# Kernel tuning notes

Hardware: AMD Instinct MI355X
Metric: run time of the kernel (lower is better)

Reference implementation:

```python
import jax, jax.numpy as jnp
import numpy as np

N_ROW = 50000
N_COL = 50000
E = 600000
D = 128
NEG_SLOPE = 0.01  # torch LeakyReLU default


def _leaky(x):
    return jnp.where(x >= 0, x, NEG_SLOPE * x)


def _mlp(x, W1, b1, W2, b2):
    # (Linear -> LeakyReLU) x2, matching nn.Sequential in Conv_layer
    h = _leaky(x @ W1 + b1)
    return _leaky(h @ W2 + b2)


def setup_inputs() -> dict:
    key = jax.random.key(0)
    ks = jax.random.split(key, 16)
    inp = {
        "feat_row": jax.random.normal(ks[0], (N_ROW, D), jnp.float32),
        "feat_col": jax.random.normal(ks[1], (N_COL, D), jnp.float32),
        "src_c2r": jax.random.randint(ks[2], (E,), 0, N_COL, jnp.int32),
        "dst_c2r": jax.random.randint(ks[3], (E,), 0, N_ROW, jnp.int32),
        "w_c2r": jax.random.uniform(ks[4], (E,), jnp.float32),
        "src_r2c": jax.random.randint(ks[5], (E,), 0, N_ROW, jnp.int32),
        "dst_r2c": jax.random.randint(ks[6], (E,), 0, N_COL, jnp.int32),
        "w_r2c": jax.random.uniform(ks[7], (E,), jnp.float32),
        "W1_c2r": jax.random.normal(ks[8], (D, D), jnp.float32) / np.sqrt(D),
        "b1_c2r": jax.random.normal(ks[9], (D,), jnp.float32) * 0.01,
        "W2_c2r": jax.random.normal(ks[10], (D, D), jnp.float32) / np.sqrt(D),
        "b2_c2r": jax.random.normal(ks[11], (D,), jnp.float32) * 0.01,
        "W1_r2c": jax.random.normal(ks[12], (D, D), jnp.float32) / np.sqrt(D),
        "b1_r2c": jax.random.normal(ks[13], (D,), jnp.float32) * 0.01,
        "W2_r2c": jax.random.normal(ks[14], (D, D), jnp.float32) / np.sqrt(D),
        "b2_r2c": jax.random.normal(ks[15], (D,), jnp.float32) * 0.01,
        "eps_c2r": jnp.zeros((), jnp.float32),  # DGL GINConv init_eps=0
        "eps_r2c": jnp.zeros((), jnp.float32),
    }
    return inp


def reference(feat_row, feat_col, src_c2r, dst_c2r, w_c2r, src_r2c, dst_r2c, w_r2c,
              W1_c2r, b1_c2r, W2_c2r, b2_c2r, W1_r2c, b1_r2c, W2_r2c, b2_r2c,
              eps_c2r, eps_r2c):
    # col -> row GINConv (edge-weighted sum aggregation)
    msg = feat_col[src_c2r] * w_c2r[:, None]                       # [E, D]
    agg_row = jax.ops.segment_sum(msg, dst_c2r, num_segments=N_ROW)
    h_row = _mlp((1.0 + eps_c2r) * feat_row + agg_row, W1_c2r, b1_c2r, W2_c2r, b2_c2r)
    # row -> col GINConv using updated row features
    msg2 = h_row[src_r2c] * w_r2c[:, None]                         # [E, D]
    agg_col = jax.ops.segment_sum(msg2, dst_r2c, num_segments=N_COL)
    h_col = _mlp((1.0 + eps_r2c) * feat_col + agg_col, W1_r2c, b1_r2c, W2_r2c, b2_r2c)
    # residual (use_residual=True): add pre-conv embeddings
    return h_row + feat_row, h_col + feat_col
```

## Files before the change

### kernel.cpp

```cpp
#include <hip/hip_runtime.h>
#include <hip/hip_bf16.h>

#define NROW 50000
#define NCOL 50000
#define DDIM 128
#define CAP  32

typedef __bf16 bf16_t;
typedef __bf16 bf16x2 __attribute__((ext_vector_type(2)));
typedef __bf16 bf16x8 __attribute__((ext_vector_type(8)));
typedef float  f32x4  __attribute__((ext_vector_type(4)));

__device__ __forceinline__ float lrelu(float v) { return v >= 0.f ? v : 0.01f * v; }

__device__ __forceinline__ float ldf(const void* p, size_t i, bool f) {
    return f ? ((const float*)p)[i] : (float)((const bf16_t*)p)[i];
}

__device__ __forceinline__ bool dtf(const int* flags, int fi) {
    return (fi == -1) ? true : (fi == -2) ? false : (flags[fi] != 0);
}

struct TensorTab { const void* p[18]; int n[18]; };

__global__ __launch_bounds__(256) void detect_zero(TensorTab T, int* flags,
                                                   int* z, int zn)
{
    const int tid = threadIdx.x;
    if (blockIdx.x >= 18) {
        int i = (blockIdx.x - 18) * 256 + tid;
        if (i < zn) z[i] = 0;
        return;
    }
    __shared__ int vb, vf;
    const int t = blockIdx.x;
    if (tid == 0) { vb = 0; vf = 0; }
    __syncthreads();
    const int n = T.n[t];
    const bool isFloatArr = (t != 2 && t != 3 && t != 5 && t != 6) && n >= 2;
    if (isFloatArr) {
        int nw = n / 2;
        int wi = (int)(((long long)tid * nw) >> 8);
        unsigned w = ((const unsigned*)T.p[t])[wi];
        unsigned low = w & 0xffffu;
        if (low) {
            int e = (int)((low >> 7) & 0xffu);
            if (e >= 90 && e <= 141) atomicAdd(&vb, 1);
            else                     atomicAdd(&vf, 1);
        }
    }
    __syncthreads();
    if (tid == 0) flags[t] = (isFloatArr && vf > vb) ? 1 : 0;
}

__device__ __forceinline__ void fill_edges(
    int e, const int* __restrict__ dst, const int* __restrict__ srcArr,
    const void* __restrict__ wArr, int nE, int* __restrict__ counts,
    int2* __restrict__ slots2, int* __restrict__ ovCnt,
    int* __restrict__ ovList, bool fW)
{
    if (e >= nE) return;
    int d = dst[e];
    int pos = atomicAdd(&counts[d], 1);
    if (pos < CAP) {
        int2 pk;
        pk.x = srcArr[e];
        pk.y = __float_as_int(ldf(wArr, e, fW));
        slots2[(size_t)d * CAP + pos] = pk;
    } else {
        int k = atomicAdd(ovCnt, 1);
        ovList[k] = e;
    }
}

struct WPtrs { const void* W[4]; int fi[4]; };

__device__ __forceinline__ void prep_one(WPtrs P, const int* flags,
                                         __bf16* wfp, int slot)
{
    if (slot >= 4 * 2048) return;
    int m = slot >> 11, sIdx = slot & 2047;
    bool f = flags[P.fi[m]] != 0;
    int l = sIdx & 63, combo = sIdx >> 6;
    int ct = combo >> 2, kk = combo & 3;
    int col  = ct * 16 + (l & 15);
    int krow = kk * 32 + (l >> 4) * 8;
    bf16x8 v;
#pragma unroll
    for (int j = 0; j < 8; ++j)
        v[j] = (__bf16)ldf(P.W[m], (size_t)(krow + j) * DDIM + col, f);
    ((bf16x8*)wfp)[slot] = v;
}

__device__ __forceinline__ void convert_one(const void* __restrict__ feat,
                                            __bf16* __restrict__ cbuf,
                                            int i, int n8, bool f)
{
    if (i >= n8) return;
    bf16x8 v;
    if (f) {
        f32x4 a = ((const f32x4*)feat)[i * 2];
        f32x4 c = ((const f32x4*)feat)[i * 2 + 1];
#pragma unroll
        for (int j = 0; j < 4; ++j) { v[j] = (__bf16)a[j]; v[j + 4] = (__bf16)c[j]; }
    } else {
        v = ((const bf16x8*)feat)[i];
    }
    ((bf16x8*)cbuf)[i] = v;
}

__global__ __launch_bounds__(1024) void prep_fill_i2(
    WPtrs P, const int* __restrict__ flags, __bf16* __restrict__ wfp,
    const void* __restrict__ feat, __bf16* __restrict__ cbuf, int n8,
    int fiFeat, int cb, int eb, int K7,
    const int* __restrict__ f_dst, const int* __restrict__ f_src,
    const void* __restrict__ f_w, int f_nE, int* __restrict__ f_counts,
    int2* __restrict__ f_slots2, int* __restrict__ f_ovCnt,
    int* __restrict__ f_ovList, int f_fiW)
{
    const int g = blockIdx.x;
    const int tid = threadIdx.x;
    if (g >= K7) {
        prep_one(P, flags, wfp, (g - K7) * 1024 + tid);
        return;
    }
    int grp = g / 7, rem = g % 7;
    if (rem < 4) {
        int b = grp * 4 + rem;
        if (b >= cb) return;
        convert_one(feat, cbuf, b * 1024 + tid, n8, dtf(flags, fiFeat));
    } else {
        int b = grp * 3 + (rem - 4);
        if (b >= eb) return;
        fill_edges(b * 1024 + tid, f_dst, f_src, f_w, f_nE, f_counts,
                   f_slots2, f_ovCnt, f_ovList, dtf(flags, f_fiW));
    }
}

__global__ __launch_bounds__(256) void segsum_fill_i(
    const __bf16* __restrict__ gsrc, const int* __restrict__ counts,
    const int2* __restrict__ slots2, float* __restrict__ agg, int nRows,
    const int* __restrict__ srcArr, const int* __restrict__ dstArr,
    const void* __restrict__ wArr, const int* __restrict__ ovList,
    const int* __restrict__ ovCount, const int* __restrict__ flags, int fiW,
    int segBlocks, int fillBlocks,
    const int* __restrict__ f_dst, const int* __restrict__ f_src,
    const void* __restrict__ f_w, int f_nE, int* __restrict__ f_counts,
    int2* __restrict__ f_slots2, int* __restrict__ f_ovCnt,
    int* __restrict__ f_ovList, int f_fiW)
{
    const int tid = threadIdx.x;
    int bid;
    if (f_dst) {
        int grp = (int)blockIdx.x / 7, rem = (int)blockIdx.x % 7;
        if (rem >= 4) {
            int b = grp * 3 + (rem - 4);
            if (b < fillBlocks)
                fill_edges(b * 256 + tid, f_dst, f_src, f_w, f_nE, f_counts,
                           f_slots2, f_ovCnt, f_ovList, dtf(flags, f_fiW));
            return;
        }
        bid = grp * 4 + rem;
        if (bid >= segBlocks) return;
    } else {
        bid = blockIdx.x;
        if (bid >= segBlocks) return;
    }

    int row = bid * 4 + (tid >> 6);
    if (row >= nRows) return;
    int lane = tid & 63;

    int cntRaw = counts[row];
    int cnt = cntRaw > CAP ? CAP : cntRaw;

    int sr = 0; float wv = 0.f;
    if (lane < cnt) {
        int2 pk = slots2[(size_t)row * CAP + lane];
        sr = pk.x;
        wv = __int_as_float(pk.y);
    }

    float2* ap = (float2*)(agg + (size_t)row * DDIM) + lane;
    float2 acc0 = {0.f, 0.f}, acc1 = {0.f, 0.f};

    const bf16x2* fb = (const bf16x2*)gsrc;
    int i = 0;
    for (; i + 4 <= cnt; i += 4) {
        int   a0 = __shfl(sr, i),     a1 = __shfl(sr, i + 1);
        int   a2 = __shfl(sr, i + 2), a3 = __shfl(sr, i + 3);
        float w0 = __shfl(wv, i),     w1 = __shfl(wv, i + 1);
        float w2 = __shfl(wv, i + 2), w3 = __shfl(wv, i + 3);
        bf16x2 v0 = fb[(size_t)a0 * 64 + lane];
        bf16x2 v1 = fb[(size_t)a1 * 64 + lane];
        bf16x2 v2 = fb[(size_t)a2 * 64 + lane];
        bf16x2 v3 = fb[(size_t)a3 * 64 + lane];
        acc0.x += (float)v0[0] * w0; acc0.y += (float)v0[1] * w0;
        acc1.x += (float)v1[0] * w1; acc1.y += (float)v1[1] * w1;
        acc0.x += (float)v2[0] * w2; acc0.y += (float)v2[1] * w2;
        acc1.x += (float)v3[0] * w3; acc1.y += (float)v3[1] * w3;
    }
    for (; i < cnt; ++i) {
        int   a0 = __shfl(sr, i);
        float w0 = __shfl(wv, i);
        bf16x2 v0 = fb[(size_t)a0 * 64 + lane];
        acc0.x += (float)v0[0] * w0; acc0.y += (float)v0[1] * w0;
    }
    if (cntRaw > CAP) {
        const bool fW = dtf(flags, fiW);
        int nOv = *ovCount;
        for (int k = 0; k < nOv; ++k) {
            int e = ovList[k];
            if (dstArr[e] == row) {
                int s = srcArr[e];
                float wf = ldf(wArr, e, fW);
                bf16x2 v = fb[(size_t)s * 64 + lane];
                acc0.x += (float)v[0] * wf; acc0.y += (float)v[1] * wf;
            }
        }
    }
    acc0.x += acc1.x; acc0.y += acc1.y;
    *ap = acc0;
}

template <bool RESIDUAL, bool HOUT>
__global__ __launch_bounds__(256) void mlp_cs(
    const void* __restrict__ feat, const float* __restrict__ agg,
    const void* __restrict__ b1, const void* __restrict__ b2,
    const void* __restrict__ epsp, float* __restrict__ out, int N,
    const int* __restrict__ flags, int fiFeat, int fiB1, int fiB2, int fiEps,
    const __bf16* __restrict__ pW1, const __bf16* __restrict__ pW2,
    __bf16* __restrict__ hout,
    int mblocks,
    const int* __restrict__ f_dst, const int* __restrict__ f_src,
    const void* __restrict__ f_w, int f_nE, int* __restrict__ f_counts,
    int2* __restrict__ f_slots2, int* __restrict__ f_ovCnt,
    int* __restrict__ f_ovList, int f_fiW)
{
    __shared__ alignas(16) __bf16 At[16 * 136];
    __shared__ alignas(16) __bf16 H1[16 * 136];

    const int tid = threadIdx.x;
    if (f_dst && (int)blockIdx.x >= mblocks) {
        int e = ((int)blockIdx.x - mblocks) * 256 + tid;
        fill_edges(e, f_dst, f_src, f_w, f_nE, f_counts, f_slots2,
                   f_ovCnt, f_ovList, dtf(flags, f_fiW));
        return;
    }

    const bool fF  = flags[fiFeat] != 0;
    const bool fB1 = flags[fiB1] != 0;
    const bool fB2 = flags[fiB2] != 0;
    const bool fE  = flags[fiEps] != 0;

    const int lane = tid & 63;
    const int wave = tid >> 6;
    const int quad = lane >> 4;
    const int r    = lane & 15;
    const int rowBase = blockIdx.x * 16;
    const float eps1 = 1.f + ldf(epsp, 0, fE);

    {
        int row = tid >> 4;
        int k0  = (tid & 15) * 8;
        int g   = rowBase + row;
        bf16x8 av;
        if (g < N) {
            size_t base = (size_t)g * DDIM + k0;
            const f32x4* gp = (const f32x4*)(agg + base);
            f32x4 g0 = gp[0], g1 = gp[1];
            if (fF) {
                const f32x4* fp = (const f32x4*)((const float*)feat + base);
                f32x4 f0 = fp[0], f1 = fp[1];
#pragma unroll
                for (int j = 0; j < 4; ++j) {
                    av[j]     = (__bf16)(f0[j] * eps1 + g0[j]);
                    av[j + 4] = (__bf16)(f1[j] * eps1 + g1[j]);
                }
            } else {
                bf16x8 fv = *(const bf16x8*)((const bf16_t*)feat + base);
#pragma unroll
                for (int j = 0; j < 4; ++j) {
                    av[j]     = (__bf16)((float)fv[j]     * eps1 + g0[j]);
                    av[j + 4] = (__bf16)((float)fv[j + 4] * eps1 + g1[j]);
                }
            }
        } else {
#pragma unroll
            for (int j = 0; j < 8; ++j) av[j] = (__bf16)0.f;
        }
        *(bf16x8*)&At[row * 136 + k0] = av;
    }
    __syncthreads();

    bf16x8 a[4];
#pragma unroll
    for (int kk = 0; kk < 4; ++kk)
        a[kk] = *(const bf16x8*)&At[r * 136 + kk * 32 + quad * 8];

    const int ct0 = wave * 2, ct1 = ct0 + 1;

    const bf16x8* pw1v = (const bf16x8*)pW1;
    bf16x8 wfa[4], wfb[4];
#pragma unroll
    for (int kk = 0; kk < 4; ++kk) {
        wfa[kk] = pw1v[(ct0 * 4 + kk) * 64 + lane];
        wfb[kk] = pw1v[(ct1 * 4 + kk) * 64 + lane];
    }
    float b1a = ldf(b1, ct0 * 16 + r, fB1);
    float b1b = ldf(b1, ct1 * 16 + r, fB1);

    {
        f32x4 acc = {0.f, 0.f, 0.f, 0.f};
#pragma unroll
        for (int kk = 0; kk < 4; ++kk)
            acc = __builtin_amdgcn_mfma_f32_16x16x32_bf16(a[kk], wfa[kk], acc, 0, 0, 0);
#pragma unroll
        for (int gg = 0; gg < 4; ++gg)
            H1[(quad * 4 + gg) * 136 + ct0 * 16 + r] = (__bf16)lrelu(acc[gg] + b1a);
    }
    {
        f32x4 acc = {0.f, 0.f, 0.f, 0.f};
#pragma unroll
        for (int kk = 0; kk < 4; ++kk)
            acc = __builtin_amdgcn_mfma_f32_16x16x32_bf16(a[kk], wfb[kk], acc, 0, 0, 0);
#pragma unroll
        for (int gg = 0; gg < 4; ++gg)
            H1[(quad * 4 + gg) * 136 + ct1 * 16 + r] = (__bf16)lrelu(acc[gg] + b1b);
    }
    __syncthreads();

    bf16x8 a2[4];
#pragma unroll
    for (int kk = 0; kk < 4; ++kk)
        a2[kk] = *(const bf16x8*)&H1[r * 136 + kk * 32 + quad * 8];

    const bf16x8* pw2v = (const bf16x8*)pW2;
#pragma unroll
    for (int kk = 0; kk < 4; ++kk) {
        wfa[kk] = pw2v[(ct0 * 4 + kk) * 64 + lane];
        wfb[kk] = pw2v[(ct1 * 4 + kk) * 64 + lane];
    }
    float b2a = ldf(b2, ct0 * 16 + r, fB2);
    float b2b = ldf(b2, ct1 * 16 + r, fB2);

#pragma unroll
    for (int cp = 0; cp < 2; ++cp) {
        const int ct = cp ? ct1 : ct0;
        f32x4 acc = {0.f, 0.f, 0.f, 0.f};
#pragma unroll
        for (int kk = 0; kk < 4; ++kk)
            acc = __builtin_amdgcn_mfma_f32_16x16x32_bf16(
                a2[kk], cp ? wfb[kk] : wfa[kk], acc, 0, 0, 0);
        float bias = cp ? b2b : b2a;
#pragma unroll
        for (int gg = 0; gg < 4; ++gg) {
            int row = rowBase + quad * 4 + gg;
            float v = lrelu(acc[gg] + bias);
            if (HOUT)
                At[(quad * 4 + gg) * 136 + ct * 16 + r] = (__bf16)v;
            if (row < N) {
                int col = ct * 16 + r;
                if (RESIDUAL) v += ldf(feat, (size_t)row * DDIM + col, fF);
                out[(size_t)row * DDIM + col] = v;
            }
        }
    }

    if (HOUT) {
        __syncthreads();
        int row = tid >> 4;
        int k0  = (tid & 15) * 8;
        int g   = rowBase + row;
        if (g < N)
            *(bf16x8*)&hout[(size_t)g * DDIM + k0] =
                *(const bf16x8*)&At[row * 136 + k0];
    }
}

__global__ __launch_bounds__(256) void prep_fill(
    WPtrs P, const int* __restrict__ flags, __bf16* __restrict__ wfp,
    const void* __restrict__ feat, __bf16* __restrict__ cbuf, int n8,
    int fiFeat, int cblocks,
    const int* __restrict__ f_dst, const int* __restrict__ f_src,
    const void* __restrict__ f_w, int f_nE, int* __restrict__ f_counts,
    int2* __restrict__ f_slots2, int* __restrict__ f_ovCnt,
    int* __restrict__ f_ovList, int f_fiW)
{
    const int b = blockIdx.x;
    const int tid = threadIdx.x;
    if (b < cblocks) {
        convert_one(feat, cbuf, b * 256 + tid, n8, dtf(flags, fiFeat));
    } else if (b < cblocks + 32) {
        prep_one(P, flags, wfp, (b - cblocks) * 256 + tid);
    } else {
        int e = (b - cblocks - 32) * 256 + tid;
        fill_edges(e, f_dst, f_src, f_w, f_nE, f_counts, f_slots2,
                   f_ovCnt, f_ovList, dtf(flags, f_fiW));
    }
}

__global__ __launch_bounds__(256) void scatter_any(
    const void* __restrict__ feat, const int* __restrict__ src,
    const int* __restrict__ dst, const void* __restrict__ w,
    float* __restrict__ agg, int nE,
    const int* __restrict__ flags, int fiFeat, int fiW)
{
    const bool fF = dtf(flags, fiFeat);
    const bool fW = dtf(flags, fiW);
    int g = blockIdx.x * 256 + threadIdx.x;
    int e = g >> 5;
    if (e >= nE) return;
    int c = (g & 31) << 2;
    int s = src[e], d = dst[e];
    float wf = ldf(w, e, fW);
    size_t base = (size_t)s * DDIM + c;
    float* ap = agg + (size_t)d * DDIM + c;
    unsafeAtomicAdd(ap + 0, ldf(feat, base + 0, fF) * wf);
    unsafeAtomicAdd(ap + 1, ldf(feat, base + 1, fF) * wf);
    unsafeAtomicAdd(ap + 2, ldf(feat, base + 2, fF) * wf);
    unsafeAtomicAdd(ap + 3, ldf(feat, base + 3, fF) * wf);
}

__global__ __launch_bounds__(256) void residual_add(
    float* __restrict__ out, const void* __restrict__ feat, int n4,
    const int* __restrict__ flags, int fiFeat)
{
    const bool fF = flags[fiFeat] != 0;
    int i = blockIdx.x * 256 + threadIdx.x;
    if (i >= n4) return;
    f32x4 o = ((const f32x4*)out)[i];
    f32x4 r;
#pragma unroll
    for (int j = 0; j < 4; ++j) r[j] = o[j] + ldf(feat, (size_t)i * 4 + j, fF);
    ((f32x4*)out)[i] = r;
}

__device__ __forceinline__ void fill_wfrag(const void* __restrict__ W, bool f,
                                           __bf16* wf, int tid)
{
#pragma unroll
    for (int i = 0; i < 8; ++i) {
        int sIdx  = tid + i * 256;
        int l     = sIdx & 63;
        int combo = sIdx >> 6;
        int ct = combo >> 2, kk = combo & 3;
        int col  = ct * 16 + (l & 15);
        int krow = kk * 32 + (l >> 4) * 8;
        __bf16* dp = wf + (size_t)sIdx * 8;
#pragma unroll
        for (int j = 0; j < 8; ++j)
            dp[j] = (__bf16)ldf(W, (size_t)(krow + j) * DDIM + col, f);
// ... 83 lines not shown
                a[kk], wv[(ct * 4 + kk) * 64 + lane], acc, 0, 0, 0);
        float bias = ldf(b1, ct * 16 + r, fB1);
#pragma unroll
        for (int gg = 0; gg < 4; ++gg)
            h1t[(wave * 16 + quad * 4 + gg) * 136 + ct * 16 + r] =
                (__bf16)lrelu(acc[gg] + bias);
    }
    __syncthreads();

    bf16x8 a2[4];
#pragma unroll
    for (int kk = 0; kk < 4; ++kk)
        a2[kk] = *(const bf16x8*)&h1t[(wave * 16 + r) * 136 + kk * 32 + quad * 8];

    fill_wfrag(W2, flags[fiW2] != 0, wf, tid);
    __syncthreads();

#pragma unroll
    for (int ct = 0; ct < 8; ++ct) {
        f32x4 acc = {0.f, 0.f, 0.f, 0.f};
#pragma unroll
        for (int kk = 0; kk < 4; ++kk)
            acc = __builtin_amdgcn_mfma_f32_16x16x32_bf16(
                a2[kk], wv[(ct * 4 + kk) * 64 + lane], acc, 0, 0, 0);
        float bias = ldf(b2, ct * 16 + r, fB2);
#pragma unroll
        for (int gg = 0; gg < 4; ++gg) {
            int row = rowBase + quad * 4 + gg;
            if (row < N) {
                int col = ct * 16 + r;
                float v = lrelu(acc[gg] + bias);
                if (RESIDUAL) v += ldf(feat, (size_t)row * DDIM + col, fF);
                out[(size_t)row * DDIM + col] = v;
            }
        }
    }
}

extern "C" void kernel_launch(void* const* d_in, const int* in_sizes, int n_in,
                              void* d_out, int out_size, void* d_ws, size_t ws_size,
                              hipStream_t stream)
{
    const int* src_c2r = (const int*)d_in[2];
    const int* dst_c2r = (const int*)d_in[3];
    const int* src_r2c = (const int*)d_in[5];
    const int* dst_r2c = (const int*)d_in[6];
    const int nE = in_sizes[2];

    char* wsb = (char*)d_ws;
    int*    flags  = (int*)wsb;
    __bf16* wfprep = (__bf16*)(wsb + 128);

    int*    cntA   = (int*)(wsb + 128 + 131072);
    int*    ovCntA = cntA + NROW;
    int*    cntB   = cntA + NROW + 8;
    int*    ovCntB = cntA + 2 * NROW + 8;
    size_t  o5 = 128 + 131072 + ((size_t)2 * NROW + 16) * 4;
    o5 = (o5 + 15) & ~(size_t)15;
    int2*   sl2A = (int2*)(wsb + o5);  o5 += (size_t)NROW * CAP * 8;
    int2*   sl2B = (int2*)(wsb + o5);  o5 += (size_t)NROW * CAP * 8;
    int*    ovLA = (int*)(wsb + o5);   o5 += (size_t)nE * 4;
    int*    ovLB = (int*)(wsb + o5);   o5 += (size_t)nE * 4;
    o5 = (o5 + 15) & ~(size_t)15;
    __bf16* cbX  = (__bf16*)(wsb + o5); o5 += (size_t)NCOL * DDIM * 2;
    __bf16* cbH  = (__bf16*)(wsb + o5); o5 += (size_t)NROW * DDIM * 2;
    const size_t NEED_A8 = o5;

    size_t  ofsA2   = 128 + 131072 + ((size_t)2 * NROW + 16) * 4;
    ofsA2 = (ofsA2 + 15) & ~(size_t)15;
    int2*   slots2A2  = (int2*)(wsb + ofsA2);
    size_t  ofsOvA2   = ofsA2 + (size_t)NROW * CAP * 8;
    int*    ovListA2  = (int*)(wsb + ofsOvA2);
    int*    ovListB2  = ovListA2 + nE;
    size_t  ofsCbA2   = (ofsOvA2 + (size_t)nE * 8 + 15) & ~(size_t)15;
    __bf16* cbufA2    = (__bf16*)(wsb + ofsCbA2);
    const size_t NEED_A2 = ofsCbA2 + (size_t)NROW * DDIM * 2;

    const bool tierA8 = ws_size >= NEED_A8;
    const bool tierA2 = ws_size >= NEED_A2;

    TensorTab T;
    for (int i = 0; i < 18; ++i) { T.p[i] = d_in[i]; T.n[i] = in_sizes[i]; }

    float* out_row = (float*)d_out;
    float* out_col = out_row + (size_t)NROW * DDIM;
    const size_t aggBytes = (size_t)NROW * DDIM * sizeof(float);

    const int eblocks  = (nE + 255) / 256;
    const int sblocks  = (nE * 32 + 255) / 256;
    const int mblocksR = (NROW + 63) / 64;
    const int mblocksC = (NCOL + 63) / 64;
    const int csR      = (NROW + 15) / 16;
    const int csC      = (NCOL + 15) / 16;
    const int gblocksR = (NROW + 3) / 4;
    const int gblocksC = (NCOL + 3) / 4;
    const int cblocks  = (NCOL * DDIM / 8 + 255) / 256;
    const int zn2      = 2 * NROW + 16;
    const int zb2      = (zn2 + 255) / 256;

    WPtrs P;
    P.W[0] = d_in[8];  P.fi[0] = 8;
    P.W[1] = d_in[10]; P.fi[1] = 10;
    P.W[2] = d_in[12]; P.fi[2] = 12;
    P.W[3] = d_in[14]; P.fi[3] = 14;

    if (tierA8) {
        const int n8  = NCOL * DDIM / 8;
        const int cb4 = (n8 + 1023) / 1024;
        const int eb4 = (nE + 1023) / 1024;
        detect_zero<<<18 + zb2, 256, 0, stream>>>(T, flags, cntA, zn2);
        {
            int ka = (cb4 + 3) / 4, kb = (eb4 + 2) / 3;
            int K = ka > kb ? ka : kb;
            prep_fill_i2<<<7 * K + 8, 1024, 0, stream>>>(
                P, flags, wfprep, d_in[1], cbX, n8, 1, cb4, eb4, 7 * K,
                dst_c2r, src_c2r, d_in[4], nE, cntA, sl2A, ovCntA, ovLA, 4);
        }
        {
            int ka = (gblocksR + 3) / 4, kb = (eblocks + 2) / 3;
            int K = ka > kb ? ka : kb;
            segsum_fill_i<<<7 * K, 256, 0, stream>>>(
                cbX, cntA, sl2A, out_col, NROW, src_c2r, dst_c2r, d_in[4],
                ovLA, ovCntA, flags, 4,
                gblocksR, eblocks, dst_r2c, src_r2c, d_in[7], nE, cntB,
                sl2B, ovCntB, ovLB, 7);
        }
        mlp_cs<true, true><<<csR, 256, 0, stream>>>(
            d_in[0], out_col, d_in[9], d_in[11], d_in[16],
            out_row, NROW, flags, 0, 9, 11, 16,
            wfprep + 0 * 16384, wfprep + 1 * 16384, cbH,
            csR, nullptr, nullptr, nullptr, 0, nullptr, nullptr,
            nullptr, nullptr, 0);
        segsum_fill_i<<<gblocksC, 256, 0, stream>>>(
            cbH, cntB, sl2B, out_col, NCOL, src_r2c, dst_r2c, d_in[7],
            ovLB, ovCntB, flags, 7,
            gblocksC, 0, nullptr, nullptr, nullptr, 0, nullptr,
            nullptr, nullptr, nullptr, 0);
        mlp_cs<true, false><<<csC, 256, 0, stream>>>(
            d_in[1], out_col, d_in[13], d_in[15], d_in[17],
            out_col, NCOL, flags, 1, 13, 15, 17,
            wfprep + 2 * 16384, wfprep + 3 * 16384, nullptr,
            csC, nullptr, nullptr, nullptr, 0, nullptr, nullptr,
            nullptr, nullptr, 0);
    } else if (tierA2) {
        detect_zero<<<18 + zb2, 256, 0, stream>>>(T, flags, cntA, zn2);
        prep_fill<<<cblocks + 32 + eblocks, 256, 0, stream>>>(
            P, flags, wfprep, d_in[1], cbufA2, NCOL * DDIM / 8, 1, cblocks,
            dst_c2r, src_c2r, d_in[4], nE, cntA, slots2A2, ovCntA,
            ovListA2, 4);
        segsum_fill_i<<<gblocksR, 256, 0, stream>>>(
            cbufA2, cntA, slots2A2, out_col, NROW, src_c2r, dst_c2r,
            d_in[4], ovListA2, ovCntA, flags, 4,
            gblocksR, 0, nullptr, nullptr, nullptr, 0, nullptr,
            nullptr, nullptr, nullptr, 0);
        mlp_cs<true, true><<<csR + eblocks, 256, 0, stream>>>(
            d_in[0], out_col, d_in[9], d_in[11], d_in[16],
            out_row, NROW, flags, 0, 9, 11, 16,
            wfprep + 0 * 16384, wfprep + 1 * 16384, cbufA2,
            csR, dst_r2c, src_r2c, d_in[7], nE, cntB, slots2A2,
            ovCntB, ovListB2, 7);
        segsum_fill_i<<<gblocksC, 256, 0, stream>>>(
            cbufA2, cntB, slots2A2, out_col, NCOL, src_r2c, dst_r2c,
            d_in[7], ovListB2, ovCntB, flags, 7,
            gblocksC, 0, nullptr, nullptr, nullptr, 0, nullptr,
            nullptr, nullptr, nullptr, 0);
        mlp_cs<true, false><<<csC, 256, 0, stream>>>(
            d_in[1], out_col, d_in[13], d_in[15], d_in[17],
            out_col, NCOL, flags, 1, 13, 15, 17,
            wfprep + 2 * 16384, wfprep + 3 * 16384, nullptr,
            csC, nullptr, nullptr, nullptr, 0, nullptr, nullptr,
            nullptr, nullptr, 0);
    } else {
        detect_zero<<<18, 256, 0, stream>>>(T, flags, nullptr, 0);
        hipMemsetAsync(out_col, 0, aggBytes, stream);
        scatter_any<<<sblocks, 256, 0, stream>>>(d_in[1], src_c2r, dst_c2r,
            d_in[4], out_col, nE, flags, 1, 4);
        mlp_kernel<false><<<mblocksR, 256, 0, stream>>>(
            d_in[0], out_col, d_in[8], d_in[9], d_in[10], d_in[11], d_in[16],
            out_row, NROW, flags, 0, 8, 9, 10, 11, 16);

        hipMemsetAsync(out_col, 0, aggBytes, stream);
        scatter_any<<<sblocks, 256, 0, stream>>>(out_row, src_r2c, dst_r2c,
            d_in[7], out_col, nE, flags, -1, 7);
        residual_add<<<(NROW * DDIM / 4 + 255) / 256, 256, 0, stream>>>(
            out_row, d_in[0], NROW * DDIM / 4, flags, 0);
        mlp_kernel<true><<<mblocksC, 256, 0, stream>>>(
            d_in[1], out_col, d_in[12], d_in[13], d_in[14], d_in[15], d_in[17],
            out_col, NCOL, flags, 1, 12, 13, 14, 15, 17);
    }
}
```

Before: 299.9 us.

## Fuse whole GIN pipeline into one cooperative persistent kernel with grid syncs

Replaces the sequence of separate launches (detect, convert/prep/fill, segment-sum/fill, MLP, segment-sum, MLP) with one cooperative persistent kernel. Grid-wide syncs separate the phases, and blocks loop over rows and tiles with grid stride. The goal is to remove per-kernel launch gaps and tail effects. In exchange, occupancy is capped at the co-resident block count, every phase waits on a full grid barrier, and the MLP phase loses the wide grid it had before. The old multi-kernel path is kept as a fallback if the cooperative launch is unavailable.

```diff
diff --git a/kernel.cpp b/kernel.cpp
--- a/kernel.cpp
+++ b/kernel.cpp
@@ -1,5 +1,8 @@
 #include <hip/hip_runtime.h>
 #include <hip/hip_bf16.h>
+#include <hip/hip_cooperative_groups.h>
+
+namespace cg = cooperative_groups;
 
 #define NROW 50000
 #define NCOL 50000
@@ -22,6 +25,378 @@
 }
 
 struct TensorTab { const void* p[18]; int n[18]; };
+struct WPtrs { const void* W[4]; int fi[4]; };
+
+__device__ __forceinline__ void fill_edges(
+    int e, const int* __restrict__ dst, const int* __restrict__ srcArr,
+    const void* __restrict__ wArr, int nE, int* __restrict__ counts,
+    int2* __restrict__ slots2, int* __restrict__ ovCnt,
+    int* __restrict__ ovList, bool fW)
+{
+    if (e >= nE) return;
+    int d = dst[e];
+    int pos = atomicAdd(&counts[d], 1);
+    if (pos < CAP) {
+        int2 pk;
+        pk.x = srcArr[e];
+        pk.y = __float_as_int(ldf(wArr, e, fW));
+        slots2[(size_t)d * CAP + pos] = pk;
+    } else {
+        int k = atomicAdd(ovCnt, 1);
+        ovList[k] = e;
+    }
+}
+
+__device__ __forceinline__ void prep_one(WPtrs P, const int* flags,
+                                         __bf16* wfp, int slot)
+{
+    if (slot >= 4 * 2048) return;
+    int m = slot >> 11, sIdx = slot & 2047;
+    bool f = flags[P.fi[m]] != 0;
+    int l = sIdx & 63, combo = sIdx >> 6;
+    int ct = combo >> 2, kk = combo & 3;
+    int col  = ct * 16 + (l & 15);
+    int krow = kk * 32 + (l >> 4) * 8;
+    bf16x8 v;
+#pragma unroll
+    for (int j = 0; j < 8; ++j)
+        v[j] = (__bf16)ldf(P.W[m], (size_t)(krow + j) * DDIM + col, f);
+    ((bf16x8*)wfp)[slot] = v;
+}
+
+__device__ __forceinline__ void convert_one(const void* __restrict__ feat,
+                                            __bf16* __restrict__ cbuf,
+                                            int i, int n8, bool f)
+{
+    if (i >= n8) return;
+    bf16x8 v;
+    if (f) {
+        f32x4 a = ((const f32x4*)feat)[i * 2];
+        f32x4 c = ((const f32x4*)feat)[i * 2 + 1];
+#pragma unroll
+        for (int j = 0; j < 4; ++j) { v[j] = (__bf16)a[j]; v[j + 4] = (__bf16)c[j]; }
+    } else {
+        v = ((const bf16x8*)feat)[i];
+    }
+    ((bf16x8*)cbuf)[i] = v;
+}
+
+__device__ void seg_rows(
+    int bid0, int strideB, const __bf16* __restrict__ gsrc,
+    const int* __restrict__ counts, const int2* __restrict__ slots2,
+    float* __restrict__ agg, int nRows,
+    const int* __restrict__ srcArr, const int* __restrict__ dstArr,
+    const void* __restrict__ wArr, const int* __restrict__ ovList,
+    const int* __restrict__ ovCount, const int* __restrict__ flags, int fiW,
+    int tid)
+{
+    const int segBlocks = (nRows + 3) >> 2;
+    const int lane = tid & 63;
+    const bf16x2* fb = (const bf16x2*)gsrc;
+    for (int b = bid0; b < segBlocks; b += strideB) {
+        int row = b * 4 + (tid >> 6);
+        if (row >= nRows) continue;
+        int cntRaw = counts[row];
+        int cnt = cntRaw > CAP ? CAP : cntRaw;
+        int sr = 0; float wv = 0.f;
+        if (lane < cnt) {
+            int2 pk = slots2[(size_t)row * CAP + lane];
+            sr = pk.x;
+            wv = __int_as_float(pk.y);
+        }
+        float2* ap = (float2*)(agg + (size_t)row * DDIM) + lane;
+        float2 acc0 = {0.f, 0.f}, acc1 = {0.f, 0.f};
+        int i = 0;
+        for (; i + 4 <= cnt; i += 4) {
+            int   a0 = __shfl(sr, i),     a1 = __shfl(sr, i + 1);
+            int   a2 = __shfl(sr, i + 2), a3 = __shfl(sr, i + 3);
+            float w0 = __shfl(wv, i),     w1 = __shfl(wv, i + 1);
+            float w2 = __shfl(wv, i + 2), w3 = __shfl(wv, i + 3);
+            bf16x2 v0 = fb[(size_t)a0 * 64 + lane];
+            bf16x2 v1 = fb[(size_t)a1 * 64 + lane];
+            bf16x2 v2 = fb[(size_t)a2 * 64 + lane];
+            bf16x2 v3 = fb[(size_t)a3 * 64 + lane];
+            acc0.x += (float)v0[0] * w0; acc0.y += (float)v0[1] * w0;
+            acc1.x += (float)v1[0] * w1; acc1.y += (float)v1[1] * w1;
+            acc0.x += (float)v2[0] * w2; acc0.y += (float)v2[1] * w2;
+            acc1.x += (float)v3[0] * w3; acc1.y += (float)v3[1] * w3;
+        }
+        for (; i < cnt; ++i) {
+            int   a0 = __shfl(sr, i);
+            float w0 = __shfl(wv, i);
+            bf16x2 v0 = fb[(size_t)a0 * 64 + lane];
+            acc0.x += (float)v0[0] * w0; acc0.y += (float)v0[1] * w0;
+        }
+        if (cntRaw > CAP) {
+            const bool fW = dtf(flags, fiW);
+            int nOv = *ovCount;
+            for (int k = 0; k < nOv; ++k) {
+                int e = ovList[k];
+                if (dstArr[e] == row) {
+                    int s = srcArr[e];
+                    float wf = ldf(wArr, e, fW);
+                    bf16x2 v = fb[(size_t)s * 64 + lane];
+                    acc0.x += (float)v[0] * wf; acc0.y += (float)v[1] * wf;
+                }
+            }
+        }
+        acc0.x += acc1.x; acc0.y += acc1.y;
+        *ap = acc0;
+    }
+}
+
+template <bool RESIDUAL, bool HOUT>
+__device__ void mlp_tiles(
+    int bid0, int strideB, __bf16* At, __bf16* H1,
+    const void* __restrict__ feat, const float* __restrict__ agg,
+    const void* __restrict__ b1, const void* __restrict__ b2,
+    const void* __restrict__ epsp, float* __restrict__ out, int N,
+    const int* __restrict__ flags, int fiFeat, int fiB1, int fiB2, int fiEps,
+    const __bf16* __restrict__ pW1, const __bf16* __restrict__ pW2,
+    __bf16* __restrict__ hout, int tid)
+{
+    const int tiles = (N + 15) >> 4;
+    const bool fF  = flags[fiFeat] != 0;
+    const bool fB1 = flags[fiB1] != 0;
+    const bool fB2 = flags[fiB2] != 0;
+    const bool fE  = flags[fiEps] != 0;
+    const int lane = tid & 63;
+    const int wave = tid >> 6;
+    const int quad = lane >> 4;
+    const int r    = lane & 15;
+    const float eps1 = 1.f + ldf(epsp, 0, fE);
+    const int ct0 = wave * 2, ct1 = ct0 + 1;
+    const bf16x8* pw1v = (const bf16x8*)pW1;
+    const bf16x8* pw2v = (const bf16x8*)pW2;
+
+    for (int b = bid0; b < tiles; b += strideB) {
+        const int rowBase = b * 16;
+        {
+            int row = tid >> 4;
+            int k0  = (tid & 15) * 8;
+            int g   = rowBase + row;
+            bf16x8 av;
+            if (g < N) {
+                size_t base = (size_t)g * DDIM + k0;
+                const f32x4* gp = (const f32x4*)(agg + base);
+                f32x4 g0 = gp[0], g1 = gp[1];
+                if (fF) {
+                    const f32x4* fp = (const f32x4*)((const float*)feat + base);
+                    f32x4 f0 = fp[0], f1 = fp[1];
+#pragma unroll
+                    for (int j = 0; j < 4; ++j) {
+                        av[j]     = (__bf16)(f0[j] * eps1 + g0[j]);
+                        av[j + 4] = (__bf16)(f1[j] * eps1 + g1[j]);
+                    }
+                } else {
+                    bf16x8 fv = *(const bf16x8*)((const bf16_t*)feat + base);
+#pragma unroll
+                    for (int j = 0; j < 4; ++j) {
+                        av[j]     = (__bf16)((float)fv[j]     * eps1 + g0[j]);
+                        av[j + 4] = (__bf16)((float)fv[j + 4] * eps1 + g1[j]);
+                    }
+                }
+            } else {
+#pragma unroll
+                for (int j = 0; j < 8; ++j) av[j] = (__bf16)0.f;
+            }
+            *(bf16x8*)&At[row * 136 + k0] = av;
+        }
+        __syncthreads();
+
+        bf16x8 a[4];
+#pragma unroll
+        for (int kk = 0; kk < 4; ++kk)
+            a[kk] = *(const bf16x8*)&At[r * 136 + kk * 32 + quad * 8];
+
+        bf16x8 wfa[4], wfb[4];
+#pragma unroll
+        for (int kk = 0; kk < 4; ++kk) {
+            wfa[kk] = pw1v[(ct0 * 4 + kk) * 64 + lane];
+            wfb[kk] = pw1v[(ct1 * 4 + kk) * 64 + lane];
+        }
+        float b1a = ldf(b1, ct0 * 16 + r, fB1);
+        float b1b = ldf(b1, ct1 * 16 + r, fB1);
+        {
+            f32x4 acc = {0.f, 0.f, 0.f, 0.f};
+#pragma unroll
+            for (int kk = 0; kk < 4; ++kk)
+                acc = __builtin_amdgcn_mfma_f32_16x16x32_bf16(a[kk], wfa[kk], acc, 0, 0, 0);
+#pragma unroll
+            for (int gg = 0; gg < 4; ++gg)
+                H1[(quad * 4 + gg) * 136 + ct0 * 16 + r] = (__bf16)lrelu(acc[gg] + b1a);
+        }
+        {
+            f32x4 acc = {0.f, 0.f, 0.f, 0.f};
+#pragma unroll
+            for (int kk = 0; kk < 4; ++kk)
+                acc = __builtin_amdgcn_mfma_f32_16x16x32_bf16(a[kk], wfb[kk], acc, 0, 0, 0);
+#pragma unroll
+            for (int gg = 0; gg < 4; ++gg)
+                H1[(quad * 4 + gg) * 136 + ct1 * 16 + r] = (__bf16)lrelu(acc[gg] + b1b);
+        }
+        __syncthreads();
+
+        bf16x8 a2[4];
+#pragma unroll
+        for (int kk = 0; kk < 4; ++kk)
+            a2[kk] = *(const bf16x8*)&H1[r * 136 + kk * 32 + quad * 8];
+
+#pragma unroll
+        for (int kk = 0; kk < 4; ++kk) {
+            wfa[kk] = pw2v[(ct0 * 4 + kk) * 64 + lane];
+            wfb[kk] = pw2v[(ct1 * 4 + kk) * 64 + lane];
+        }
+        float b2a = ldf(b2, ct0 * 16 + r, fB2);
+        float b2b = ldf(b2, ct1 * 16 + r, fB2);
+
+#pragma unroll
+        for (int cp = 0; cp < 2; ++cp) {
+            const int ct = cp ? ct1 : ct0;
+            f32x4 acc = {0.f, 0.f, 0.f, 0.f};
+#pragma unroll
+            for (int kk = 0; kk < 4; ++kk)
+                acc = __builtin_amdgcn_mfma_f32_16x16x32_bf16(
+                    a2[kk], cp ? wfb[kk] : wfa[kk], acc, 0, 0, 0);
+            float bias = cp ? b2b : b2a;
+#pragma unroll
+            for (int gg = 0; gg < 4; ++gg) {
+                int row = rowBase + quad * 4 + gg;
+                float v = lrelu(acc[gg] + bias);
+                if (HOUT)
+                    At[(quad * 4 + gg) * 136 + ct * 16 + r] = (__bf16)v;
+                if (row < N) {
+                    int col = ct * 16 + r;
+                    if (RESIDUAL) v += ldf(feat, (size_t)row * DDIM + col, fF);
+                    out[(size_t)row * DDIM + col] = v;
+                }
+            }
+        }
+
+        if (HOUT) {
+            __syncthreads();
+            int row = tid >> 4;
+            int k0  = (tid & 15) * 8;
+            int g   = rowBase + row;
+            if (g < N)
+                *(bf16x8*)&hout[(size_t)g * DDIM + k0] =
+                    *(const bf16x8*)&At[row * 136 + k0];
+        }
+        __syncthreads();
+    }
+}
+
+struct MegaArgs {
+    TensorTab T;
+    WPtrs P;
+    int* flags;
+    __bf16* wfp;
+    const void* featRow;
+    const void* featCol;
+    __bf16* cbX;
+    __bf16* cbH;
+    const int* srcA; const int* dstA; const void* wA;
+    const int* srcB; const int* dstB; const void* wB;
+    int nE;
+    int* cntA; int* cntB;
+    int2* sl2A; int2* sl2B;
+    int* ovLA; int* ovLB;
+    float* out_row; float* out_col;
+    const void* b1A; const void* b2A; const void* epsA;
+    const void* b1B; const void* b2B; const void* epsB;
+    int zn; int n8;
+};
+
+__global__ __launch_bounds__(256, 8) void mega(MegaArgs A)
+{
+    cg::grid_group grid = cg::this_grid();
+    __shared__ alignas(16) __bf16 At[16 * 136];
+    __shared__ alignas(16) __bf16 H1[16 * 136];
+    __shared__ int vb, vf;
+
+    const int tid = threadIdx.x;
+    const int bid = (int)blockIdx.x;
+    const int nB  = (int)gridDim.x;
+    const int gthreads = nB * 256;
+    const int g = bid * 256 + tid;
+
+    for (int i = g; i < A.zn; i += gthreads) A.cntA[i] = 0;
+    if (bid < 18) {
+        const int t = bid;
+        if (tid == 0) { vb = 0; vf = 0; }
+        __syncthreads();
+        const int n = A.T.n[t];
+        const bool isFloatArr = (t != 2 && t != 3 && t != 5 && t != 6) && n >= 2;
+        if (isFloatArr) {
+            int nw = n / 2;
+            int wi = (int)(((long long)tid * nw) >> 8);
+            unsigned w = ((const unsigned*)A.T.p[t])[wi];
+            unsigned low = w & 0xffffu;
+            if (low) {
+                int e = (int)((low >> 7) & 0xffu);
+                if (e >= 90 && e <= 141) atomicAdd(&vb, 1);
+                else                     atomicAdd(&vf, 1);
+            }
+        }
+        __syncthreads();
+        if (tid == 0) A.flags[t] = (isFloatArr && vf > vb) ? 1 : 0;
+    }
+    grid.sync();
+
+    {
+        int C = (nB * 4) / 7;
+        if (C < 1) C = 1;
+        if (C >= nB) C = nB - 1;
+        if (bid < C) {
+            int lg = bid * 256 + tid, lt = C * 256;
+            bool fX = dtf(A.flags, 1);
+            for (int i = lg; i < A.n8; i += lt)
+                convert_one(A.featCol, A.cbX, i, A.n8, fX);
+            for (int s = lg; s < 4 * 2048; s += lt)
+                prep_one(A.P, A.flags, A.wfp, s);
+        } else {
+            int lg = (bid - C) * 256 + tid, lt = (nB - C) * 256;
+            bool fW = dtf(A.flags, 4);
+            for (int e = lg; e < A.nE; e += lt)
+                fill_edges(e, A.dstA, A.srcA, A.wA, A.nE, A.cntA, A.sl2A,
+                           A.cntA + NROW, A.ovLA, fW);
+        }
+    }
+    grid.sync();
+
+    {
+        int S = (nB * 4) / 7;
+        if (S < 1) S = 1;
+        if (S >= nB) S = nB - 1;
+        if (bid < S) {
+            seg_rows(bid, S, A.cbX, A.cntA, A.sl2A, A.out_col, NROW,
+                     A.srcA, A.dstA, A.wA, A.ovLA, A.cntA + NROW,
+                     A.flags, 4, tid);
+        } else {
+            int lg = (bid - S) * 256 + tid, lt = (nB - S) * 256;
+            bool fW = dtf(A.flags, 7);
+            for (int e = lg; e < A.nE; e += lt)
+                fill_edges(e, A.dstB, A.srcB, A.wB, A.nE, A.cntB, A.sl2B,
+                           A.cntB + NROW, A.ovLB, fW);
+        }
+    }
+    grid.sync();
+
+    mlp_tiles<true, true>(bid, nB, At, H1, A.featRow, A.out_col,
+                          A.b1A, A.b2A, A.epsA, A.out_row, NROW,
+                          A.flags, 0, 9, 11, 16,
+                          A.wfp + 0 * 16384, A.wfp + 1 * 16384, A.cbH, tid);
+    grid.sync();
+
+    seg_rows(bid, nB, A.cbH, A.cntB, A.sl2B, A.out_col, NCOL,
+             A.srcB, A.dstB, A.wB, A.ovLB, A.cntB + NROW, A.flags, 7, tid);
+    grid.sync();
+
+    mlp_tiles<true, false>(bid, nB, At, H1, A.featCol, A.out_col,
+                           A.b1B, A.b2B, A.epsB, A.out_col, NCOL,
+                           A.flags, 1, 13, 15, 17,
+                           A.wfp + 2 * 16384, A.wfp + 3 * 16384, nullptr, tid);
+}
 
 __global__ __launch_bounds__(256) void detect_zero(TensorTab T, int* flags,
                                                    int* z, int zn)
@@ -53,62 +428,6 @@
     if (tid == 0) flags[t] = (isFloatArr && vf > vb) ? 1 : 0;
 }
 
-__device__ __forceinline__ void fill_edges(
-    int e, const int* __restrict__ dst, const int* __restrict__ srcArr,
-    const void* __restrict__ wArr, int nE, int* __restrict__ counts,
-    int2* __restrict__ slots2, int* __restrict__ ovCnt,
-    int* __restrict__ ovList, bool fW)
-{
-    if (e >= nE) return;
-    int d = dst[e];
-    int pos = atomicAdd(&counts[d], 1);
-    if (pos < CAP) {
-        int2 pk;
-        pk.x = srcArr[e];
-        pk.y = __float_as_int(ldf(wArr, e, fW));
-        slots2[(size_t)d * CAP + pos] = pk;
-    } else {
-        int k = atomicAdd(ovCnt, 1);
-        ovList[k] = e;
-    }
-}
-
-struct WPtrs { const void* W[4]; int fi[4]; };
-
-__device__ __forceinline__ void prep_one(WPtrs P, const int* flags,
-                                         __bf16* wfp, int slot)
-{
-    if (slot >= 4 * 2048) return;
-    int m = slot >> 11, sIdx = slot & 2047;
-    bool f = flags[P.fi[m]] != 0;
-    int l = sIdx & 63, combo = sIdx >> 6;
-    int ct = combo >> 2, kk = combo & 3;
-    int col  = ct * 16 + (l & 15);
-    int krow = kk * 32 + (l >> 4) * 8;
-    bf16x8 v;
-#pragma unroll
-    for (int j = 0; j < 8; ++j)
-        v[j] = (__bf16)ldf(P.W[m], (size_t)(krow + j) * DDIM + col, f);
-    ((bf16x8*)wfp)[slot] = v;
-}
-
-__device__ __forceinline__ void convert_one(const void* __restrict__ feat,
-                                            __bf16* __restrict__ cbuf,
-                                            int i, int n8, bool f)
-{
-    if (i >= n8) return;
-    bf16x8 v;
-    if (f) {
-        f32x4 a = ((const f32x4*)feat)[i * 2];
-        f32x4 c = ((const f32x4*)feat)[i * 2 + 1];
-#pragma unroll
-        for (int j = 0; j < 4; ++j) { v[j] = (__bf16)a[j]; v[j + 4] = (__bf16)c[j]; }
-    } else {
-        v = ((const bf16x8*)feat)[i];
-    }
-    ((bf16x8*)cbuf)[i] = v;
-}
-
 __global__ __launch_bounds__(1024) void prep_fill_i2(
     WPtrs P, const int* __restrict__ flags, __bf16* __restrict__ wfp,
     const void* __restrict__ feat, __bf16* __restrict__ cbuf, int n8,
@@ -166,61 +485,8 @@
         bid = blockIdx.x;
         if (bid >= segBlocks) return;
     }
-
-    int row = bid * 4 + (tid >> 6);
-    if (row >= nRows) return;
-    int lane = tid & 63;
-
-    int cntRaw = counts[row];
-    int cnt = cntRaw > CAP ? CAP : cntRaw;
-
-    int sr = 0; float wv = 0.f;
-    if (lane < cnt) {
-        int2 pk = slots2[(size_t)row * CAP + lane];
-        sr = pk.x;
-        wv = __int_as_float(pk.y);
-    }
-
-    float2* ap = (float2*)(agg + (size_t)row * DDIM) + lane;
-    float2 acc0 = {0.f, 0.f}, acc1 = {0.f, 0.f};
-
-    const bf16x2* fb = (const bf16x2*)gsrc;
-    int i = 0;
-    for (; i + 4 <= cnt; i += 4) {
-        int   a0 = __shfl(sr, i),     a1 = __shfl(sr, i + 1);
-        int   a2 = __shfl(sr, i + 2), a3 = __shfl(sr, i + 3);
-        float w0 = __shfl(wv, i),     w1 = __shfl(wv, i + 1);
-        float w2 = __shfl(wv, i + 2), w3 = __shfl(wv, i + 3);
-        bf16x2 v0 = fb[(size_t)a0 * 64 + lane];
-        bf16x2 v1 = fb[(size_t)a1 * 64 + lane];
-        bf16x2 v2 = fb[(size_t)a2 * 64 + lane];
-        bf16x2 v3 = fb[(size_t)a3 * 64 + lane];
-        acc0.x += (float)v0[0] * w0; acc0.y += (float)v0[1] * w0;
-        acc1.x += (float)v1[0] * w1; acc1.y += (float)v1[1] * w1;
-        acc0.x += (float)v2[0] * w2; acc0.y += (float)v2[1] * w2;
-        acc1.x += (float)v3[0] * w3; acc1.y += (float)v3[1] * w3;
-    }
-    for (; i < cnt; ++i) {
-        int   a0 = __shfl(sr, i);
-        float w0 = __shfl(wv, i);
-        bf16x2 v0 = fb[(size_t)a0 * 64 + lane];
-        acc0.x += (float)v0[0] * w0; acc0.y += (float)v0[1] * w0;
-    }
-    if (cntRaw > CAP) {
-        const bool fW = dtf(flags, fiW);
-        int nOv = *ovCount;
-        for (int k = 0; k < nOv; ++k) {
-            int e = ovList[k];
-            if (dstArr[e] == row) {
-                int s = srcArr[e];
-                float wf = ldf(wArr, e, fW);
-                bf16x2 v = fb[(size_t)s * 64 + lane];
-                acc0.x += (float)v[0] * wf; acc0.y += (float)v[1] * wf;
-            }
-        }
-    }
-    acc0.x += acc1.x; acc0.y += acc1.y;
-    *ap = acc0;
+    seg_rows(bid, 0x40000000, gsrc, counts, slots2, agg, nRows, srcArr,
+             dstArr, wArr, ovList, ovCount, flags, fiW, tid);
 }
 
 template <bool RESIDUAL, bool HOUT>
@@ -239,7 +505,6 @@
 {
     __shared__ alignas(16) __bf16 At[16 * 136];
     __shared__ alignas(16) __bf16 H1[16 * 136];
-
     const int tid = threadIdx.x;
     if (f_dst && (int)blockIdx.x >= mblocks) {
         int e = ((int)blockIdx.x - mblocks) * 256 + tid;
@@ -247,157 +512,10 @@
                    f_ovCnt, f_ovList, dtf(flags, f_fiW));
         return;
     }
-
-    const bool fF  = flags[fiFeat] != 0;
-    const bool fB1 = flags[fiB1] != 0;
-    const bool fB2 = flags[fiB2] != 0;
-    const bool fE  = flags[fiEps] != 0;
-
-    const int lane = tid & 63;
-    const int wave = tid >> 6;
-    const int quad = lane >> 4;
-    const int r    = lane & 15;
-    const int rowBase = blockIdx.x * 16;
-    const float eps1 = 1.f + ldf(epsp, 0, fE);
-
-    {
-        int row = tid >> 4;
-        int k0  = (tid & 15) * 8;
-        int g   = rowBase + row;
-        bf16x8 av;
-        if (g < N) {
-            size_t base = (size_t)g * DDIM + k0;
-            const f32x4* gp = (const f32x4*)(agg + base);
-            f32x4 g0 = gp[0], g1 = gp[1];
-            if (fF) {
-                const f32x4* fp = (const f32x4*)((const float*)feat + base);
-                f32x4 f0 = fp[0], f1 = fp[1];
-#pragma unroll
-                for (int j = 0; j < 4; ++j) {
-                    av[j]     = (__bf16)(f0[j] * eps1 + g0[j]);
-                    av[j + 4] = (__bf16)(f1[j] * eps1 + g1[j]);
-                }
-            } else {
-                bf16x8 fv = *(const bf16x8*)((const bf16_t*)feat + base);
-#pragma unroll
-                for (int j = 0; j < 4; ++j) {
-                    av[j]     = (__bf16)((float)fv[j]     * eps1 + g0[j]);
-                    av[j + 4] = (__bf16)((float)fv[j + 4] * eps1 + g1[j]);
-                }
-            }
-        } else {
-#pragma unroll
-            for (int j = 0; j < 8; ++j) av[j] = (__bf16)0.f;
-        }
-        *(bf16x8*)&At[row * 136 + k0] = av;
-    }
-    __syncthreads();
-
-    bf16x8 a[4];
-#pragma unroll
-    for (int kk = 0; kk < 4; ++kk)
-        a[kk] = *(const bf16x8*)&At[r * 136 + kk * 32 + quad * 8];
-
-    const int ct0 = wave * 2, ct1 = ct0 + 1;
-
-    const bf16x8* pw1v = (const bf16x8*)pW1;
-    bf16x8 wfa[4], wfb[4];
-#pragma unroll
-    for (int kk = 0; kk < 4; ++kk) {
-        wfa[kk] = pw1v[(ct0 * 4 + kk) * 64 + lane];
-        wfb[kk] = pw1v[(ct1 * 4 + kk) * 64 + lane];
-    }
-    float b1a = ldf(b1, ct0 * 16 + r, fB1);
-    float b1b = ldf(b1, ct1 * 16 + r, fB1);
-
-    {
-        f32x4 acc = {0.f, 0.f, 0.f, 0.f};
-#pragma unroll
-        for (int kk = 0; kk < 4; ++kk)
-            acc = __builtin_amdgcn_mfma_f32_16x16x32_bf16(a[kk], wfa[kk], acc, 0, 0, 0);
-#pragma unroll
-        for (int gg = 0; gg < 4; ++gg)
-            H1[(quad * 4 + gg) * 136 + ct0 * 16 + r] = (__bf16)lrelu(acc[gg] + b1a);
-    }
-    {
-        f32x4 acc = {0.f, 0.f, 0.f, 0.f};
-#pragma unroll
-        for (int kk = 0; kk < 4; ++kk)
-            acc = __builtin_amdgcn_mfma_f32_16x16x32_bf16(a[kk], wfb[kk], acc, 0, 0, 0);
-#pragma unroll
-        for (int gg = 0; gg < 4; ++gg)
-            H1[(quad * 4 + gg) * 136 + ct1 * 16 + r] = (__bf16)lrelu(acc[gg] + b1b);
-    }
-    __syncthreads();
-
-    bf16x8 a2[4];
-#pragma unroll
-    for (int kk = 0; kk < 4; ++kk)
-        a2[kk] = *(const bf16x8*)&H1[r * 136 + kk * 32 + quad * 8];
-
-    const bf16x8* pw2v = (const bf16x8*)pW2;
-#pragma unroll
-    for (int kk = 0; kk < 4; ++kk) {
-        wfa[kk] = pw2v[(ct0 * 4 + kk) * 64 + lane];
-        wfb[kk] = pw2v[(ct1 * 4 + kk) * 64 + lane];
-    }
-    float b2a = ldf(b2, ct0 * 16 + r, fB2);
-    float b2b = ldf(b2, ct1 * 16 + r, fB2);
-
-#pragma unroll
-    for (int cp = 0; cp < 2; ++cp) {
-        const int ct = cp ? ct1 : ct0;
-        f32x4 acc = {0.f, 0.f, 0.f, 0.f};
-#pragma unroll
-        for (int kk = 0; kk < 4; ++kk)
-            acc = __builtin_amdgcn_mfma_f32_16x16x32_bf16(
-                a2[kk], cp ? wfb[kk] : wfa[kk], acc, 0, 0, 0);
-        float bias = cp ? b2b : b2a;
-#pragma unroll
-        for (int gg = 0; gg < 4; ++gg) {
-            int row = rowBase + quad * 4 + gg;
-            float v = lrelu(acc[gg] + bias);
-            if (HOUT)
-                At[(quad * 4 + gg) * 136 + ct * 16 + r] = (__bf16)v;
-            if (row < N) {
-                int col = ct * 16 + r;
-                if (RESIDUAL) v += ldf(feat, (size_t)row * DDIM + col, fF);
-                out[(size_t)row * DDIM + col] = v;
-            }
-        }
-    }
-
-    if (HOUT) {
-        __syncthreads();
-        int row = tid >> 4;
-        int k0  = (tid & 15) * 8;
-        int g   = rowBase + row;
-        if (g < N)
-            *(bf16x8*)&hout[(size_t)g * DDIM + k0] =
-                *(const bf16x8*)&At[row * 136 + k0];
-    }
-}
-
-__global__ __launch_bounds__(256) void prep_fill(
-    WPtrs P, const int* __restrict__ flags, __bf16* __restrict__ wfp,
-    const void* __restrict__ feat, __bf16* __restrict__ cbuf, int n8,
-    int fiFeat, int cblocks,
-    const int* __restrict__ f_dst, const int* __restrict__ f_src,
-    const void* __restrict__ f_w, int f_nE, int* __restrict__ f_counts,
-    int2* __restrict__ f_slots2, int* __restrict__ f_ovCnt,
-    int* __restrict__ f_ovList, int f_fiW)
-{
-    const int b = blockIdx.x;
-    const int tid = threadIdx.x;
-    if (b < cblocks) {
-        convert_one(feat, cbuf, b * 256 + tid, n8, dtf(flags, fiFeat));
-    } else if (b < cblocks + 32) {
-        prep_one(P, flags, wfp, (b - cblocks) * 256 + tid);
-    } else {
-        int e = (b - cblocks - 32) * 256 + tid;
-        fill_edges(e, f_dst, f_src, f_w, f_nE, f_counts, f_slots2,
-                   f_ovCnt, f_ovList, dtf(flags, f_fiW));
-    }
+    if ((int)blockIdx.x >= mblocks) return;
+    mlp_tiles<RESIDUAL, HOUT>((int)blockIdx.x, 0x40000000, At, H1, feat, agg,
+                              b1, b2, epsp, out, N, flags,
+                              fiFeat, fiB1, fiB2, fiEps, pW1, pW2, hout, tid);
 }
 
 __global__ __launch_bounds__(256) void scatter_any(
@@ -587,9 +705,7 @@
     __bf16* wfprep = (__bf16*)(wsb + 128);
 
     int*    cntA   = (int*)(wsb + 128 + 131072);
-    int*    ovCntA = cntA + NROW;
     int*    cntB   = cntA + NROW + 8;
-    int*    ovCntB = cntA + 2 * NROW + 8;
     size_t  o5 = 128 + 131072 + ((size_t)2 * NROW + 16) * 4;
     o5 = (o5 + 15) & ~(size_t)15;
     int2*   sl2A = (int2*)(wsb + o5);  o5 += (size_t)NROW * CAP * 8;
@@ -600,19 +716,7 @@
     __bf16* cbX  = (__bf16*)(wsb + o5); o5 += (size_t)NCOL * DDIM * 2;
     __bf16* cbH  = (__bf16*)(wsb + o5); o5 += (size_t)NROW * DDIM * 2;
     const size_t NEED_A8 = o5;
-
-    size_t  ofsA2   = 128 + 131072 + ((size_t)2 * NROW + 16) * 4;
-    ofsA2 = (ofsA2 + 15) & ~(size_t)15;
-    int2*   slots2A2  = (int2*)(wsb + ofsA2);
-    size_t  ofsOvA2   = ofsA2 + (size_t)NROW * CAP * 8;
-    int*    ovListA2  = (int*)(wsb + ofsOvA2);
-    int*    ovListB2  = ovListA2 + nE;
-    size_t  ofsCbA2   = (ofsOvA2 + (size_t)nE * 8 + 15) & ~(size_t)15;
-    __bf16* cbufA2    = (__bf16*)(wsb + ofsCbA2);
-    const size_t NEED_A2 = ofsCbA2 + (size_t)NROW * DDIM * 2;
-
     const bool tierA8 = ws_size >= NEED_A8;
-    const bool tierA2 = ws_size >= NEED_A2;
 
     TensorTab T;
     for (int i = 0; i < 18; ++i) { T.p[i] = d_in[i]; T.n[i] = in_sizes[i]; }
@@ -629,7 +733,6 @@
     const int csC      = (NCOL + 15) / 16;
     const int gblocksR = (NROW + 3) / 4;
     const int gblocksC = (NCOL + 3) / 4;
-    const int cblocks  = (NCOL * DDIM / 8 + 255) / 256;
     const int zn2      = 2 * NROW + 16;
     const int zb2      = (zn2 + 255) / 256;
 
@@ -638,6 +741,37 @@
     P.W[1] = d_in[10]; P.fi[1] = 10;
     P.W[2] = d_in[12]; P.fi[2] = 12;
     P.W[3] = d_in[14]; P.fi[3] = 14;
+
+    if (tierA8) {
+        int coopAttr = 0, nCU = 0, maxB = 0;
+        hipDeviceGetAttribute(&coopAttr, hipDeviceAttributeCooperativeLaunch, 0);
+        hipDeviceGetAttribute(&nCU, hipDeviceAttributeMultiprocessorCount, 0);
+        hipOccupancyMaxActiveBlocksPerMultiprocessor(&maxB, (const void*)mega,
+                                                     256, 0);
+        if (coopAttr && nCU > 0 && maxB > 0 && (long long)maxB * nCU >= 64) {
+            MegaArgs A;
+            A.T = T; A.P = P;
+            A.flags = flags; A.wfp = wfprep;
+            A.featRow = d_in[0]; A.featCol = d_in[1];
+            A.cbX = cbX; A.cbH = cbH;
+            A.srcA = src_c2r; A.dstA = dst_c2r; A.wA = d_in[4];
+            A.srcB = src_r2c; A.dstB = dst_r2c; A.wB = d_in[7];
+            A.nE = nE;
+            A.cntA = cntA; A.cntB = cntB;
+            A.sl2A = sl2A; A.sl2B = sl2B;
+            A.ovLA = ovLA; A.ovLB = ovLB;
+            A.out_row = out_row; A.out_col = out_col;
+            A.b1A = d_in[9];  A.b2A = d_in[11]; A.epsA = d_in[16];
+            A.b1B = d_in[13]; A.b2B = d_in[15]; A.epsB = d_in[17];
+            A.zn = zn2; A.n8 = NCOL * DDIM / 8;
+            void* kargs[] = { (void*)&A };
+            hipError_t err = hipLaunchCooperativeKernel(
+                (const void*)mega, dim3((unsigned)(maxB * nCU)), dim3(256),
+                kargs, 0, stream);
+            if (err == hipSuccess) return;
+            (void)hipGetLastError();
+        }
+    }
 
     if (tierA8) {
         const int n8  = NCOL * DDIM / 8;
@@ -649,16 +783,16 @@
             int K = ka > kb ? ka : kb;
             prep_fill_i2<<<7 * K + 8, 1024, 0, stream>>>(
                 P, flags, wfprep, d_in[1], cbX, n8, 1, cb4, eb4, 7 * K,
-                dst_c2r, src_c2r, d_in[4], nE, cntA, sl2A, ovCntA, ovLA, 4);
+                dst_c2r, src_c2r, d_in[4], nE, cntA, sl2A, cntA + NROW, ovLA, 4);
         }
         {
             int ka = (gblocksR + 3) / 4, kb = (eblocks + 2) / 3;
             int K = ka > kb ? ka : kb;
             segsum_fill_i<<<7 * K, 256, 0, stream>>>(
                 cbX, cntA, sl2A, out_col, NROW, src_c2r, dst_c2r, d_in[4],
-                ovLA, ovCntA, flags, 4,
+                ovLA, cntA + NROW, flags, 4,
                 gblocksR, eblocks, dst_r2c, src_r2c, d_in[7], nE, cntB,
-                sl2B, ovCntB, ovLB, 7);
+                sl2B, cntB + NROW, ovLB, 7);
         }
         mlp_cs<true, true><<<csR, 256, 0, stream>>>(
             d_in[0], out_col, d_in[9], d_in[11], d_in[16],
@@ -668,35 +802,7 @@
             nullptr, nullptr, 0);
         segsum_fill_i<<<gblocksC, 256, 0, stream>>>(
             cbH, cntB, sl2B, out_col, NCOL, src_r2c, dst_r2c, d_in[7],
-            ovLB, ovCntB, flags, 7,
-            gblocksC, 0, nullptr, nullptr, nullptr, 0, nullptr,
-            nullptr, nullptr, nullptr, 0);
-        mlp_cs<true, false><<<csC, 256, 0, stream>>>(
-            d_in[1], out_col, d_in[13], d_in[15], d_in[17],
-            out_col, NCOL, flags, 1, 13, 15, 17,
-            wfprep + 2 * 16384, wfprep + 3 * 16384, nullptr,
-            csC, nullptr, nullptr, nullptr, 0, nullptr, nullptr,
-            nullptr, nullptr, 0);
-    } else if (tierA2) {
-        detect_zero<<<18 + zb2, 256, 0, stream>>>(T, flags, cntA, zn2);
-        prep_fill<<<cblocks + 32 + eblocks, 256, 0, stream>>>(
-            P, flags, wfprep, d_in[1], cbufA2, NCOL * DDIM / 8, 1, cblocks,
-            dst_c2r, src_c2r, d_in[4], nE, cntA, slots2A2, ovCntA,
-            ovListA2, 4);
-        segsum_fill_i<<<gblocksR, 256, 0, stream>>>(
-            cbufA2, cntA, slots2A2, out_col, NROW, src_c2r, dst_c2r,
-            d_in[4], ovListA2, ovCntA, flags, 4,
-            gblocksR, 0, nullptr, nullptr, nullptr, 0, nullptr,
-            nullptr, nullptr, nullptr, 0);
-        mlp_cs<true, true><<<csR + eblocks, 256, 0, stream>>>(
-            d_in[0], out_col, d_in[9], d_in[11], d_in[16],
-            out_row, NROW, flags, 0, 9, 11, 16,
-            wfprep + 0 * 16384, wfprep + 1 * 16384, cbufA2,
-            csR, dst_r2c, src_r2c, d_in[7], nE, cntB, slots2A2,
-            ovCntB, ovListB2, 7);
-        segsum_fill_i<<<gblocksC, 256, 0, stream>>>(
-            cbufA2, cntB, slots2A2, out_col, NCOL, src_r2c, dst_r2c,
-            d_in[7], ovListB2, ovCntB, flags, 7,
+            ovLB, cntB + NROW, flags, 7,
             gblocksC, 0, nullptr, nullptr, nullptr, 0, nullptr,
             nullptr, nullptr, nullptr, 0);
         mlp_cs<true, false><<<csC, 256, 0, stream>>>(
```

Measured after the change: 1.099 ms. +266.6%, slower.
